# Kernel tuning notes

Measured on AMD Instinct MI355X. Metric: run time of the kernel, lower is better.

The kernel has to match this reference:

```python
import jax, jax.numpy as jnp
import numpy as np


def setup_inputs() -> dict:
    key = jax.random.key(0)
    ks = jax.random.split(key, 12)
    b, S, c, d = 2, 20, 256, 4
    sc = 0.05

    def w(k, shape):
        return jax.random.normal(k, shape, jnp.float32) * sc

    return {
        "x": jax.random.normal(ks[0], (b, S, c, d, d), jnp.float32),
        "W1": w(ks[1], (2 * (c + 2), 256)), "b1": jnp.zeros((256,), jnp.float32),
        "W2": w(ks[2], (256, 256)), "b2": jnp.zeros((256,), jnp.float32),
        "W3": w(ks[3], (256, 256)), "b3": jnp.zeros((256,), jnp.float32),
        "W4": w(ks[4], (256, 256)), "b4": jnp.zeros((256,), jnp.float32),
        "Wf1": w(ks[5], (256, 256)), "bf1": jnp.zeros((256,), jnp.float32),
        "Wf2": w(ks[6], (256, 256)), "bf2": jnp.zeros((256,), jnp.float32),
        "Wf3": w(ks[7], (256, 29)), "bf3": jnp.zeros((29,), jnp.float32),
        "Wf4": w(ks[8], (29, 1)), "bf4": jnp.zeros((1,), jnp.float32),
    }


def reference(x, W1, b1, W2, b2, W3, b3, W4, b4,
              Wf1, bf1, Wf2, bf2, Wf3, bf3, Wf4, bf4):
    # x: [b, S, c, d, d] post-repnet features
    b, S, c, d, _ = x.shape
    cc = c + 2  # feature channels after coord concat
    # coord[0,i,j] = i/d, coord[1,i,j] = j/d (matches torch transpose chain)
    r = jnp.arange(d, dtype=x.dtype) / d
    coord = jnp.stack(jnp.meshgrid(r, r, indexing="ij"), axis=0)  # [2, d, d]
    xc = jnp.concatenate(
        [x, jnp.broadcast_to(coord, (b, S, 2, d, d))], axis=2)     # [b,S,cc,d,d]
    xf = xc.reshape(b, S, cc, d * d).transpose(0, 1, 3, 2)         # [b,S,P,cc]

    # First g layer on concat([x_i, x_j]) == split W1 and broadcast-add.
    # Pair feature at (b, s1, s2, p1, p2) = [x[b,s2,:,p2], x[b,s1,:,p1]].
    A = jnp.einsum("bspc,ch->bsph", xf, W1[:cc])   # x_i contribution
    B = jnp.einsum("bspc,ch->bsph", xf, W1[cc:])   # x_j contribution
    h = jax.nn.relu(A[:, None, :, None, :, :] + B[:, :, None, :, None, :] + b1)
    # h: [b, S, S, P, P, 256]
    h = jax.nn.relu(h @ W2 + b2)
    h = jax.nn.relu(h @ W3 + b3)
    h = jax.nn.relu(h @ W4 + b4)
    pooled = h.sum(axis=(3, 4))                    # [b, S, S, 256]

    y = jax.nn.relu(pooled @ Wf1 + bf1)
    y = jax.nn.relu(y @ Wf2 + bf2)  # Dropout is identity in eval/reference
    y = jax.nn.relu(y @ Wf3 + bf3)
    score = jax.nn.sigmoid(y @ Wf4 + bf4)[..., 0]  # [b, S, S]
    return score
```

## Files before the change

kernel.cpp:

```cpp
#include <hip/hip_runtime.h>
#include <hip/hip_bf16.h>
#include <math.h>

typedef _Float16 f16x8 __attribute__((ext_vector_type(8)));
typedef _Float16 f16x4 __attribute__((ext_vector_type(4)));
typedef float f32x4 __attribute__((ext_vector_type(4)));

#define LDH 264

__global__ void prep(const float* __restrict__ x, const float* __restrict__ W1,
                     const float* __restrict__ b1,
                     const float* __restrict__ W2, const float* __restrict__ W3,
                     const float* __restrict__ W4,
                     float* __restrict__ A, float* __restrict__ B,
                     _Float16* __restrict__ Wt) {
    if (blockIdx.x < 48) {
        __shared__ _Float16 ws[256 * 17];
        int L = blockIdx.x >> 4, cg = blockIdx.x & 15;
        const float* W = (L == 0) ? W2 : (L == 1) ? W3 : W4;
        int t = threadIdx.x;
        for (int i = t; i < 4096; i += 512) {
            int k = i >> 4, c = i & 15;
            ws[k * 17 + c] = (_Float16)W[k * 256 + cg * 16 + c];
        }
        __syncthreads();
        int l = t >> 3, e = t & 7;
        int c = l & 15, kb = (l >> 4) * 8 + e;
        _Float16* dst = Wt + (size_t)((L * 16 + cg) * 8) * 512 + t;
#pragma unroll
        for (int kk = 0; kk < 8; kk++)
            dst[kk * 512] = ws[(kk * 32 + kb) * 17 + c];
        return;
    }
    __shared__ float xs[258 * 4];
    int blk = blockIdx.x - 48;
    int bs = blk >> 2, pg = blk & 3;
    for (int i = threadIdx.x; i < 1024; i += 512) {
        int c = i >> 2, pp = i & 3;
        xs[i] = x[bs * 4096 + c * 16 + pg * 4 + pp];
    }
    if (threadIdx.x < 8) {
        int pp = threadIdx.x & 3, c = 256 + (threadIdx.x >> 2);
        int p = pg * 4 + pp;
        xs[c * 4 + pp] = (float)((c == 256) ? (p >> 2) : (p & 3)) * 0.25f;
    }
    __syncthreads();
    int half = threadIdx.x >> 8;
    int col  = threadIdx.x & 255;
    float acc[4] = {0.f, 0.f, 0.f, 0.f};
    const float* Wp = W1 + half * 258 * 256 + col;
#pragma unroll 1
    for (int c0 = 0; c0 < 256; c0 += 8) {
        float w[8];
#pragma unroll
        for (int j = 0; j < 8; j++) w[j] = Wp[(c0 + j) * 256];
#pragma unroll
        for (int j = 0; j < 8; j++)
#pragma unroll
            for (int pp = 0; pp < 4; pp++) acc[pp] += xs[(c0 + j) * 4 + pp] * w[j];
    }
#pragma unroll
    for (int c = 256; c < 258; c++) {
        float w = Wp[c * 256];
#pragma unroll
        for (int pp = 0; pp < 4; pp++) acc[pp] += xs[c * 4 + pp] * w;
    }
    float* out = half ? B : A;
    float bias = half ? 0.f : b1[col];
#pragma unroll
    for (int pp = 0; pp < 4; pp++)
        out[(bs * 16 + pg * 4 + pp) * 256 + col] = acc[pp] + bias;
}

__global__ __launch_bounds__(256, 3) void pairnet(
        const float* __restrict__ A, const float* __restrict__ B,
        const _Float16* __restrict__ Wt,
        const float* __restrict__ b2, const float* __restrict__ b3,
        const float* __restrict__ b4, float* __restrict__ pooled4) {
    __shared__ _Float16 hb[64 * LDH];

    int blk = blockIdx.x;
    int qtr = blk & 3;
    int bss = blk >> 2;
    int s2  = bss % 20;
    int s1  = (bss / 20) % 20;
    int b   = bss / 400;
    int tid = threadIdx.x;

    const float* Abase = A + (b * 20 + s2) * 16 * 256;
    const float* Bbase = B + ((b * 20 + s1) * 16 + qtr * 4) * 256;
#pragma unroll
    for (int it = 0; it < 8; it++) {
        int u = it * 256 + tid;
        int r = u >> 5;
        int c = (u & 31) * 8;
        const float* Ap = Abase + (r & 15) * 256 + c;
        const float* Bp = Bbase + (r >> 4) * 256 + c;
        float4 a0 = *(const float4*)(Ap);
        float4 a1 = *(const float4*)(Ap + 4);
        float4 b0 = *(const float4*)(Bp);
        float4 b1 = *(const float4*)(Bp + 4);
        f16x8 hv;
        hv[0] = (_Float16)fmaxf(a0.x + b0.x, 0.f);
        hv[1] = (_Float16)fmaxf(a0.y + b0.y, 0.f);
        hv[2] = (_Float16)fmaxf(a0.z + b0.z, 0.f);
        hv[3] = (_Float16)fmaxf(a0.w + b0.w, 0.f);
        hv[4] = (_Float16)fmaxf(a1.x + b1.x, 0.f);
        hv[5] = (_Float16)fmaxf(a1.y + b1.y, 0.f);
        hv[6] = (_Float16)fmaxf(a1.z + b1.z, 0.f);
        hv[7] = (_Float16)fmaxf(a1.w + b1.w, 0.f);
        *(f16x8*)(hb + r * LDH + c) = hv;
    }
    __syncthreads();

    int wid = tid >> 6, lane = tid & 63;
    int col0 = wid * 64;
    int lr = lane & 15, lk = lane >> 4;

#pragma unroll
    for (int L = 0; L < 3; L++) {
        const float* bias = (L == 0) ? b2 : (L == 1) ? b3 : b4;
        const _Float16* wb = Wt + (size_t)((L * 16 + wid * 4) * 8) * 512 + lane * 8;

        f32x4 acc[4][4];
#pragma unroll
        for (int m = 0; m < 4; m++)
#pragma unroll
            for (int n = 0; n < 4; n++) acc[m][n] = (f32x4){0.f, 0.f, 0.f, 0.f};

#pragma unroll
        for (int kk = 0; kk < 8; kk++) {
            f16x8 w[4], a[4];
#pragma unroll
            for (int n = 0; n < 4; n++)
                w[n] = *(const f16x8*)(wb + (n * 8 + kk) * 512);
#pragma unroll
            for (int m = 0; m < 4; m++)
                a[m] = *(const f16x8*)(hb + (16 * m + lr) * LDH + kk * 32 + 8 * lk);
#pragma unroll
            for (int m = 0; m < 4; m++)
#pragma unroll
                for (int n = 0; n < 4; n++)
                    acc[m][n] = __builtin_amdgcn_mfma_f32_16x16x32_f16(
                        w[n], a[m], acc[m][n], 0, 0, 0);
        }

        if (L < 2) {
            __syncthreads();
#pragma unroll
            for (int n = 0; n < 4; n++) {
                int cb = col0 + 16 * n + 4 * lk;
                float4 b4v = *(const float4*)(bias + cb);
#pragma unroll
                for (int m = 0; m < 4; m++) {
                    int row = 16 * m + lr;
                    f16x4 hv;
                    hv[0] = (_Float16)fmaxf(acc[m][n][0] + b4v.x, 0.f);
                    hv[1] = (_Float16)fmaxf(acc[m][n][1] + b4v.y, 0.f);
                    hv[2] = (_Float16)fmaxf(acc[m][n][2] + b4v.z, 0.f);
                    hv[3] = (_Float16)fmaxf(acc[m][n][3] + b4v.w, 0.f);
                    *(f16x4*)(hb + row * LDH + cb) = hv;
                }
            }
            __syncthreads();
        } else {
#pragma unroll
            for (int n = 0; n < 4; n++) {
                int cb = col0 + 16 * n + 4 * lk;
                float4 b4v = *(const float4*)(bias + cb);
                f32x4 s = (f32x4){0.f, 0.f, 0.f, 0.f};
#pragma unroll
                for (int m = 0; m < 4; m++) {
                    s[0] += fmaxf(acc[m][n][0] + b4v.x, 0.f);
                    s[1] += fmaxf(acc[m][n][1] + b4v.y, 0.f);
                    s[2] += fmaxf(acc[m][n][2] + b4v.z, 0.f);
                    s[3] += fmaxf(acc[m][n][3] + b4v.w, 0.f);
                }
#pragma unroll
                for (int mask = 1; mask <= 8; mask <<= 1) {
#pragma unroll
                    for (int c = 0; c < 4; c++) s[c] += __shfl_xor(s[c], mask);
                }
                if (lr == 0) {
                    float4 sv; sv.x = s[0]; sv.y = s[1]; sv.z = s[2]; sv.w = s[3];
                    *(float4*)(pooled4 + ((size_t)qtr * 800 + bss) * 256 + cb) = sv;
                }
            }
        }
    }
}

__global__ void final_mlp(const float* __restrict__ pooled4,
        const float* __restrict__ Wf1, const float* __restrict__ bf1,
        const float* __restrict__ Wf2, const float* __restrict__ bf2,
        const float* __restrict__ Wf3, const float* __restrict__ bf3,
        const float* __restrict__ Wf4, const float* __restrict__ bf4,
        float* __restrict__ out) {
    __shared__ float p[4][256], y[4][256], z[4][256], y3[4][29];
    int r0 = blockIdx.x * 4;
    int t  = threadIdx.x;
    for (int i = t; i < 1024; i += 256) {
        int r = i >> 8, c = i & 255;
        float v = 0.f;
#pragma unroll
        for (int q = 0; q < 4; q++)
            v += pooled4[((size_t)q * 800 + r0 + r) * 256 + c];
        p[r][c] = v;
    }
    __syncthreads();
    float acc[4];
#pragma unroll
    for (int r = 0; r < 4; r++) acc[r] = bf1[t];
#pragma unroll 1
    for (int k0 = 0; k0 < 256; k0 += 8) {
        float w[8];
#pragma unroll
        for (int j = 0; j < 8; j++) w[j] = Wf1[(k0 + j) * 256 + t];
#pragma unroll
        for (int j = 0; j < 8; j++)
#pragma unroll
            for (int r = 0; r < 4; r++) acc[r] += p[r][k0 + j] * w[j];
    }
#pragma unroll
    for (int r = 0; r < 4; r++) y[r][t] = fmaxf(acc[r], 0.f);
    __syncthreads();
#pragma unroll
    for (int r = 0; r < 4; r++) acc[r] = bf2[t];
#pragma unroll 1
    for (int k0 = 0; k0 < 256; k0 += 8) {
        float w[8];
#pragma unroll
        for (int j = 0; j < 8; j++) w[j] = Wf2[(k0 + j) * 256 + t];
#pragma unroll
        for (int j = 0; j < 8; j++)
#pragma unroll
            for (int r = 0; r < 4; r++) acc[r] += y[r][k0 + j] * w[j];
    }
#pragma unroll
    for (int r = 0; r < 4; r++) z[r][t] = fmaxf(acc[r], 0.f);
    __syncthreads();
    if (t < 116) {
        int r = t / 29, c = t % 29;
        float a = bf3[c];
#pragma unroll 1
        for (int k0 = 0; k0 < 256; k0 += 8) {
            float w[8];
#pragma unroll
            for (int j = 0; j < 8; j++) w[j] = Wf3[(k0 + j) * 29 + c];
#pragma unroll
            for (int j = 0; j < 8; j++) a += z[r][k0 + j] * w[j];
        }
        y3[r][c] = fmaxf(a, 0.f);
    }
    __syncthreads();
    if (t < 4) {
        float zz = bf4[0];
#pragma unroll
        for (int c = 0; c < 29; c++) zz += y3[t][c] * Wf4[c];
        out[r0 + t] = 1.f / (1.f + expf(-zz));
    }
}

extern "C" void kernel_launch(void* const* d_in, const int* in_sizes, int n_in,
                              void* d_out, int out_size, void* d_ws, size_t ws_size,
                              hipStream_t stream) {
    const float* x   = (const float*)d_in[0];
    const float* W1  = (const float*)d_in[1];
    const float* b1  = (const float*)d_in[2];
    const float* W2  = (const float*)d_in[3];
    const float* b2  = (const float*)d_in[4];
    const float* W3  = (const float*)d_in[5];
    const float* b3  = (const float*)d_in[6];
    const float* W4  = (const float*)d_in[7];
    const float* b4  = (const float*)d_in[8];
    const float* Wf1 = (const float*)d_in[9];
    const float* bf1 = (const float*)d_in[10];
    const float* Wf2 = (const float*)d_in[11];
    const float* bf2 = (const float*)d_in[12];
    const float* Wf3 = (const float*)d_in[13];
    const float* bf3 = (const float*)d_in[14];
    const float* Wf4 = (const float*)d_in[15];
    const float* bf4 = (const float*)d_in[16];

    float* A       = (float*)d_ws;
    float* B       = A + 640 * 256;
    float* pooled4 = B + 640 * 256;
    _Float16* Wt   = (_Float16*)(pooled4 + 4 * 800 * 256);

    prep<<<208, 512, 0, stream>>>(x, W1, b1, W2, W3, W4, A, B, Wt);
    pairnet<<<3200, 256, 0, stream>>>(A, B, Wt, b2, b3, b4, pooled4);
    final_mlp<<<200, 256, 0, stream>>>(pooled4, Wf1, bf1, Wf2, bf2, Wf3, bf3, Wf4, bf4,
                                       (float*)d_out);
}
```

Before: 122.6 us.

## Shrink pairnet blocks, store A/B in fp16, atomically pool, widen final MLP

A and B are now stored as fp16, and the first-layer add plus ReLU is done with packed half arithmetic. pairnet runs 6400 blocks of 128 threads, each handling 32 rows with a 2x8 MFMA tile per wave. Bias is folded into the accumulator init, and partial pooled sums are combined with atomicAdd into a single buffer that a memset zeroes first. final_mlp processes 8 rows per block with 512 threads and splits K across two halves. This cuts global traffic and LDS per block so more blocks fit, at the cost of fp16 rounding of A/B, atomic contention and an extra memset.

Result: slower. 201.6 us (+64.5%).

```diff
diff --git a/kernel.cpp b/kernel.cpp
--- a/kernel.cpp
+++ b/kernel.cpp
@@ -12,7 +12,7 @@
                      const float* __restrict__ b1,
                      const float* __restrict__ W2, const float* __restrict__ W3,
                      const float* __restrict__ W4,
-                     float* __restrict__ A, float* __restrict__ B,
+                     _Float16* __restrict__ A, _Float16* __restrict__ B,
                      _Float16* __restrict__ Wt) {
     if (blockIdx.x < 48) {
         __shared__ _Float16 ws[256 * 17];
@@ -65,82 +65,76 @@
 #pragma unroll
         for (int pp = 0; pp < 4; pp++) acc[pp] += xs[c * 4 + pp] * w;
     }
-    float* out = half ? B : A;
+    _Float16* out = half ? B : A;
     float bias = half ? 0.f : b1[col];
 #pragma unroll
     for (int pp = 0; pp < 4; pp++)
-        out[(bs * 16 + pg * 4 + pp) * 256 + col] = acc[pp] + bias;
-}
-
-__global__ __launch_bounds__(256, 3) void pairnet(
-        const float* __restrict__ A, const float* __restrict__ B,
+        out[(bs * 16 + pg * 4 + pp) * 256 + col] = (_Float16)(acc[pp] + bias);
+}
+
+__global__ __launch_bounds__(128, 4) void pairnet(
+        const _Float16* __restrict__ A, const _Float16* __restrict__ B,
         const _Float16* __restrict__ Wt,
         const float* __restrict__ b2, const float* __restrict__ b3,
-        const float* __restrict__ b4, float* __restrict__ pooled4) {
-    __shared__ _Float16 hb[64 * LDH];
+        const float* __restrict__ b4, float* __restrict__ pooled) {
+    __shared__ _Float16 hb[32 * LDH];
 
     int blk = blockIdx.x;
-    int qtr = blk & 3;
-    int bss = blk >> 2;
+    int g   = blk & 7;
+    int bss = blk >> 3;
     int s2  = bss % 20;
     int s1  = (bss / 20) % 20;
     int b   = bss / 400;
     int tid = threadIdx.x;
 
-    const float* Abase = A + (b * 20 + s2) * 16 * 256;
-    const float* Bbase = B + ((b * 20 + s1) * 16 + qtr * 4) * 256;
+    const _Float16* Abase = A + (b * 20 + s2) * 16 * 256;
+    const _Float16* Bbase = B + ((b * 20 + s1) * 16 + g * 2) * 256;
 #pragma unroll
     for (int it = 0; it < 8; it++) {
-        int u = it * 256 + tid;
+        int u = it * 128 + tid;
         int r = u >> 5;
         int c = (u & 31) * 8;
-        const float* Ap = Abase + (r & 15) * 256 + c;
-        const float* Bp = Bbase + (r >> 4) * 256 + c;
-        float4 a0 = *(const float4*)(Ap);
-        float4 a1 = *(const float4*)(Ap + 4);
-        float4 b0 = *(const float4*)(Bp);
-        float4 b1 = *(const float4*)(Bp + 4);
-        f16x8 hv;
-        hv[0] = (_Float16)fmaxf(a0.x + b0.x, 0.f);
-        hv[1] = (_Float16)fmaxf(a0.y + b0.y, 0.f);
-        hv[2] = (_Float16)fmaxf(a0.z + b0.z, 0.f);
-        hv[3] = (_Float16)fmaxf(a0.w + b0.w, 0.f);
-        hv[4] = (_Float16)fmaxf(a1.x + b1.x, 0.f);
-        hv[5] = (_Float16)fmaxf(a1.y + b1.y, 0.f);
-        hv[6] = (_Float16)fmaxf(a1.z + b1.z, 0.f);
-        hv[7] = (_Float16)fmaxf(a1.w + b1.w, 0.f);
+        f16x8 av = *(const f16x8*)(Abase + (r & 15) * 256 + c);
+        f16x8 bv = *(const f16x8*)(Bbase + (r >> 4) * 256 + c);
+        f16x8 hv = av + bv;
+#pragma unroll
+        for (int j = 0; j < 8; j++)
+            hv[j] = hv[j] > (_Float16)0.f ? hv[j] : (_Float16)0.f;
         *(f16x8*)(hb + r * LDH + c) = hv;
     }
     __syncthreads();
 
     int wid = tid >> 6, lane = tid & 63;
-    int col0 = wid * 64;
+    int col0 = wid * 128;
     int lr = lane & 15, lk = lane >> 4;
 
 #pragma unroll
     for (int L = 0; L < 3; L++) {
         const float* bias = (L == 0) ? b2 : (L == 1) ? b3 : b4;
-        const _Float16* wb = Wt + (size_t)((L * 16 + wid * 4) * 8) * 512 + lane * 8;
-
-        f32x4 acc[4][4];
-#pragma unroll
-        for (int m = 0; m < 4; m++)
-#pragma unroll
-            for (int n = 0; n < 4; n++) acc[m][n] = (f32x4){0.f, 0.f, 0.f, 0.f};
+        const _Float16* wb = Wt + (size_t)((L * 16 + wid * 8) * 8) * 512 + lane * 8;
+
+        f32x4 acc[2][8];
+#pragma unroll
+        for (int n = 0; n < 8; n++) {
+            int cb = col0 + 16 * n + 4 * lk;
+            float4 bv = *(const float4*)(bias + cb);
+            f32x4 iv; iv[0] = bv.x; iv[1] = bv.y; iv[2] = bv.z; iv[3] = bv.w;
+            acc[0][n] = iv; acc[1][n] = iv;
+        }
 
 #pragma unroll
         for (int kk = 0; kk < 8; kk++) {
-            f16x8 w[4], a[4];
-#pragma unroll
-            for (int n = 0; n < 4; n++)
+            f16x8 w[8], a[2];
+#pragma unroll
+            for (int n = 0; n < 8; n++)
                 w[n] = *(const f16x8*)(wb + (n * 8 + kk) * 512);
 #pragma unroll
-            for (int m = 0; m < 4; m++)
+            for (int m = 0; m < 2; m++)
                 a[m] = *(const f16x8*)(hb + (16 * m + lr) * LDH + kk * 32 + 8 * lk);
 #pragma unroll
-            for (int m = 0; m < 4; m++)
-#pragma unroll
-                for (int n = 0; n < 4; n++)
+            for (int m = 0; m < 2; m++)
+#pragma unroll
+                for (int n = 0; n < 8; n++)
                     acc[m][n] = __builtin_amdgcn_mfma_f32_16x16x32_f16(
                         w[n], a[m], acc[m][n], 0, 0, 0);
         }
@@ -148,98 +142,103 @@
         if (L < 2) {
             __syncthreads();
 #pragma unroll
-            for (int n = 0; n < 4; n++) {
+            for (int n = 0; n < 8; n++) {
                 int cb = col0 + 16 * n + 4 * lk;
-                float4 b4v = *(const float4*)(bias + cb);
-#pragma unroll
-                for (int m = 0; m < 4; m++) {
+#pragma unroll
+                for (int m = 0; m < 2; m++) {
                     int row = 16 * m + lr;
                     f16x4 hv;
-                    hv[0] = (_Float16)fmaxf(acc[m][n][0] + b4v.x, 0.f);
-                    hv[1] = (_Float16)fmaxf(acc[m][n][1] + b4v.y, 0.f);
-                    hv[2] = (_Float16)fmaxf(acc[m][n][2] + b4v.z, 0.f);
-                    hv[3] = (_Float16)fmaxf(acc[m][n][3] + b4v.w, 0.f);
+                    hv[0] = (_Float16)fmaxf(acc[m][n][0], 0.f);
+                    hv[1] = (_Float16)fmaxf(acc[m][n][1], 0.f);
+                    hv[2] = (_Float16)fmaxf(acc[m][n][2], 0.f);
+                    hv[3] = (_Float16)fmaxf(acc[m][n][3], 0.f);
                     *(f16x4*)(hb + row * LDH + cb) = hv;
                 }
             }
             __syncthreads();
         } else {
 #pragma unroll
-            for (int n = 0; n < 4; n++) {
+            for (int n = 0; n < 8; n++) {
                 int cb = col0 + 16 * n + 4 * lk;
-                float4 b4v = *(const float4*)(bias + cb);
-                f32x4 s = (f32x4){0.f, 0.f, 0.f, 0.f};
-#pragma unroll
-                for (int m = 0; m < 4; m++) {
-                    s[0] += fmaxf(acc[m][n][0] + b4v.x, 0.f);
-                    s[1] += fmaxf(acc[m][n][1] + b4v.y, 0.f);
-                    s[2] += fmaxf(acc[m][n][2] + b4v.z, 0.f);
-                    s[3] += fmaxf(acc[m][n][3] + b4v.w, 0.f);
-                }
+                f32x4 s;
+#pragma unroll
+                for (int j = 0; j < 4; j++)
+                    s[j] = fmaxf(acc[0][n][j], 0.f) + fmaxf(acc[1][n][j], 0.f);
 #pragma unroll
                 for (int mask = 1; mask <= 8; mask <<= 1) {
 #pragma unroll
-                    for (int c = 0; c < 4; c++) s[c] += __shfl_xor(s[c], mask);
+                    for (int j = 0; j < 4; j++) s[j] += __shfl_xor(s[j], mask);
                 }
                 if (lr == 0) {
-                    float4 sv; sv.x = s[0]; sv.y = s[1]; sv.z = s[2]; sv.w = s[3];
-                    *(float4*)(pooled4 + ((size_t)qtr * 800 + bss) * 256 + cb) = sv;
+                    float* pp = pooled + (size_t)bss * 256 + cb;
+#pragma unroll
+                    for (int j = 0; j < 4; j++) atomicAdd(pp + j, s[j]);
                 }
             }
         }
     }
 }
 
-__global__ void final_mlp(const float* __restrict__ pooled4,
+__global__ void final_mlp(const float* __restrict__ pooled,
         const float* __restrict__ Wf1, const float* __restrict__ bf1,
         const float* __restrict__ Wf2, const float* __restrict__ bf2,
         const float* __restrict__ Wf3, const float* __restrict__ bf3,
         const float* __restrict__ Wf4, const float* __restrict__ bf4,
         float* __restrict__ out) {
-    __shared__ float p[4][256], y[4][256], z[4][256], y3[4][29];
-    int r0 = blockIdx.x * 4;
+    __shared__ float p[8][256], ps[2][8][256], yb[8][256], zb[8][256], y3[8][29];
+    int r0 = blockIdx.x * 8;
     int t  = threadIdx.x;
-    for (int i = t; i < 1024; i += 256) {
-        int r = i >> 8, c = i & 255;
-        float v = 0.f;
-#pragma unroll
-        for (int q = 0; q < 4; q++)
-            v += pooled4[((size_t)q * 800 + r0 + r) * 256 + c];
-        p[r][c] = v;
-    }
-    __syncthreads();
-    float acc[4];
-#pragma unroll
-    for (int r = 0; r < 4; r++) acc[r] = bf1[t];
-#pragma unroll 1
-    for (int k0 = 0; k0 < 256; k0 += 8) {
+    int kh = t >> 8, col = t & 255;
+    for (int i = t; i < 2048; i += 512)
+        p[i >> 8][i & 255] = pooled[(size_t)r0 * 256 + i];
+    __syncthreads();
+
+    float acc[8];
+#pragma unroll
+    for (int r = 0; r < 8; r++) acc[r] = 0.f;
+#pragma unroll 1
+    for (int k0 = kh * 128; k0 < kh * 128 + 128; k0 += 8) {
         float w[8];
 #pragma unroll
-        for (int j = 0; j < 8; j++) w[j] = Wf1[(k0 + j) * 256 + t];
-#pragma unroll
-        for (int j = 0; j < 8; j++)
-#pragma unroll
-            for (int r = 0; r < 4; r++) acc[r] += p[r][k0 + j] * w[j];
-    }
-#pragma unroll
-    for (int r = 0; r < 4; r++) y[r][t] = fmaxf(acc[r], 0.f);
-    __syncthreads();
-#pragma unroll
-    for (int r = 0; r < 4; r++) acc[r] = bf2[t];
-#pragma unroll 1
-    for (int k0 = 0; k0 < 256; k0 += 8) {
+        for (int j = 0; j < 8; j++) w[j] = Wf1[(k0 + j) * 256 + col];
+#pragma unroll
+        for (int j = 0; j < 8; j++)
+#pragma unroll
+            for (int r = 0; r < 8; r++) acc[r] += p[r][k0 + j] * w[j];
+    }
+#pragma unroll
+    for (int r = 0; r < 8; r++) ps[kh][r][col] = acc[r];
+    __syncthreads();
+    if (t < 256) {
+#pragma unroll
+        for (int r = 0; r < 8; r++)
+            yb[r][t] = fmaxf(ps[0][r][t] + ps[1][r][t] + bf1[t], 0.f);
+    }
+    __syncthreads();
+
+#pragma unroll
+    for (int r = 0; r < 8; r++) acc[r] = 0.f;
+#pragma unroll 1
+    for (int k0 = kh * 128; k0 < kh * 128 + 128; k0 += 8) {
         float w[8];
 #pragma unroll
-        for (int j = 0; j < 8; j++) w[j] = Wf2[(k0 + j) * 256 + t];
-#pragma unroll
-        for (int j = 0; j < 8; j++)
-#pragma unroll
-            for (int r = 0; r < 4; r++) acc[r] += y[r][k0 + j] * w[j];
-    }
-#pragma unroll
-    for (int r = 0; r < 4; r++) z[r][t] = fmaxf(acc[r], 0.f);
-    __syncthreads();
-    if (t < 116) {
+        for (int j = 0; j < 8; j++) w[j] = Wf2[(k0 + j) * 256 + col];
+#pragma unroll
+        for (int j = 0; j < 8; j++)
+#pragma unroll
+            for (int r = 0; r < 8; r++) acc[r] += yb[r][k0 + j] * w[j];
+    }
+#pragma unroll
+    for (int r = 0; r < 8; r++) ps[kh][r][col] = acc[r];
+    __syncthreads();
+    if (t < 256) {
+#pragma unroll
+        for (int r = 0; r < 8; r++)
+            zb[r][t] = fmaxf(ps[0][r][t] + ps[1][r][t] + bf2[t], 0.f);
+    }
+    __syncthreads();
+
+    if (t < 232) {
         int r = t / 29, c = t % 29;
         float a = bf3[c];
 #pragma unroll 1
@@ -248,12 +247,12 @@
 #pragma unroll
             for (int j = 0; j < 8; j++) w[j] = Wf3[(k0 + j) * 29 + c];
 #pragma unroll
-            for (int j = 0; j < 8; j++) a += z[r][k0 + j] * w[j];
+            for (int j = 0; j < 8; j++) a += zb[r][k0 + j] * w[j];
         }
         y3[r][c] = fmaxf(a, 0.f);
     }
     __syncthreads();
-    if (t < 4) {
+    if (t < 8) {
         float zz = bf4[0];
 #pragma unroll
         for (int c = 0; c < 29; c++) zz += y3[t][c] * Wf4[c];
@@ -282,13 +281,14 @@
     const float* Wf4 = (const float*)d_in[15];
     const float* bf4 = (const float*)d_in[16];
 
-    float* A       = (float*)d_ws;
-    float* B       = A + 640 * 256;
-    float* pooled4 = B + 640 * 256;
-    _Float16* Wt   = (_Float16*)(pooled4 + 4 * 800 * 256);
-
-    prep<<<208, 512, 0, stream>>>(x, W1, b1, W2, W3, W4, A, B, Wt);
-    pairnet<<<3200, 256, 0, stream>>>(A, B, Wt, b2, b3, b4, pooled4);
-    final_mlp<<<200, 256, 0, stream>>>(pooled4, Wf1, bf1, Wf2, bf2, Wf3, bf3, Wf4, bf4,
-                                       (float*)d_out);
-}
+    float* pooled = (float*)d_ws;
+    _Float16* A   = (_Float16*)(pooled + 800 * 256);
+    _Float16* Bp  = A + 640 * 256;
+    _Float16* Wt  = Bp + 640 * 256;
+
+    hipMemsetAsync(pooled, 0, 800 * 256 * sizeof(float), stream);
+    prep<<<208, 512, 0, stream>>>(x, W1, b1, W2, W3, W4, A, Bp, Wt);
+    pairnet<<<6400, 128, 0, stream>>>(A, Bp, Wt, b2, b3, b4, pooled);
+    final_mlp<<<100, 512, 0, stream>>>(pooled, Wf1, bf1, Wf2, bf2, Wf3, bf3,
+                                       Wf4, bf4, (float*)d_out);
+}
```
